# Performance work log

Hardware: AMD Instinct MI355X
Metric: run time of the kernel (lower is better)

Reference implementation:

```python
import jax, jax.numpy as jnp
import numpy as np

LMAX = 8
RES_BETA = 32   # Gauss-Legendre points in beta (>= 2*LMAX+1 -> exact quadrature for product)
RES_ALPHA = 63  # uniform points in alpha (>= 2*(2*LMAX)+1)
BATCH = 16384
DIM = (LMAX + 1) ** 2  # 81 real SH coefficients, flat index i = l*l + l + m


def _normalized_assoc_legendre(lmax, y):
    # P[b, l, m] = orthonormalized associated Legendre \bar{P}_l^m(y), 0<=m<=l,
    # normalized so that int_{-1}^{1} Pbar_l^m Pbar_l'^m dy = delta_{ll'} / (2*pi).
    n = len(y)
    P = np.zeros((n, lmax + 1, lmax + 1))
    sx = np.sqrt(np.clip(1.0 - y * y, 0.0, None))
    P[:, 0, 0] = np.sqrt(1.0 / (4.0 * np.pi))
    for m in range(1, lmax + 1):
        P[:, m, m] = -np.sqrt((2.0 * m + 1.0) / (2.0 * m)) * sx * P[:, m - 1, m - 1]
    for m in range(lmax):
        P[:, m + 1, m] = np.sqrt(2.0 * m + 3.0) * y * P[:, m, m]
    for m in range(lmax + 1):
        for l in range(m + 2, lmax + 1):
            a = np.sqrt((4.0 * l * l - 1.0) / (l * l - m * m))
            b = np.sqrt(((l - 1.0) ** 2 - m * m) / (4.0 * (l - 1.0) ** 2 - 1.0))
            P[:, l, m] = a * (y * P[:, l - 1, m] - b * P[:, l - 2, m])
    return P


def _s2grid_basis():
    # Gauss-Legendre nodes y=cos(beta) and weights (integrate sin(beta) d(beta) exactly)
    y, w = np.polynomial.legendre.leggauss(RES_BETA)
    P = _normalized_assoc_legendre(LMAX, y)
    alphas = 2.0 * np.pi * np.arange(RES_ALPHA) / RES_ALPHA
    shb = np.zeros((RES_BETA, DIM))   # Legendre part, per flat (l,m) index
    sha = np.zeros((RES_ALPHA, DIM))  # Fourier part, per flat (l,m) index
    s2 = np.sqrt(2.0)
    for l in range(LMAX + 1):
        for m in range(-l, l + 1):
            i = l * l + l + m
            shb[:, i] = P[:, l, abs(m)]
            if m == 0:
                sha[:, i] = 1.0
            elif m > 0:
                sha[:, i] = s2 * np.cos(m * alphas)
            else:
                sha[:, i] = s2 * np.sin(-m * alphas)
    qw = w * (2.0 * np.pi / RES_ALPHA)  # combined beta quadrature + alpha trapezoid weight
    return (shb.astype(np.float32), sha.astype(np.float32), qw.astype(np.float32))


def setup_inputs() -> dict:
    key = jax.random.key(0)
    k1, k2 = jax.random.split(key)
    shb, sha, qw = _s2grid_basis()
    return {
        "input1": jax.random.normal(k1, (BATCH, DIM), dtype=jnp.float32),
        "input2": jax.random.normal(k2, (BATCH, DIM), dtype=jnp.float32),
        "shb": jnp.asarray(shb),
        "sha": jnp.asarray(sha),
        "qw": jnp.asarray(qw),
    }


def _to_s2grid(x, shb, sha):
    # x: [Z, D] -> grid: [Z, res_beta, res_alpha]
    t = jnp.einsum('zi,bi->zbi', x, shb)        # Legendre expansion along beta
    return jnp.einsum('zbi,ai->zba', t, sha)    # Fourier synthesis along alpha


def _from_s2grid(g, shb, sha, qw):
    # g: [Z, res_beta, res_alpha] -> coeffs: [Z, D]
    t = jnp.einsum('zba,ai->zbi', g, sha)       # Fourier analysis along alpha
    return jnp.einsum('zbi,bi,b->zi', t, shb, qw)  # Legendre projection with quadrature


def reference(input1, input2, shb, sha, qw):
    g1 = _to_s2grid(input1, shb, sha)
    g2 = _to_s2grid(input2, shb, sha)
    return _from_s2grid(g1 * g2, shb, sha, qw)
```

## Files before the change

### kernel.cpp

```cpp
#include <hip/hip_runtime.h>

#define DIM 81
#define RA  63
#define RB  32
#define ZT  32
#define XS  104
#define OS  100

#define OFF_SHAA 0
#define OFF_SHAT 12288
#define OFF_SHBH 24576
#define OFF_SHBQ 30720
#define WS_NEED  43008

#define L_XP      43008
#define L_OB      56320
#define LDS_BYTES 69120

typedef _Float16 half8 __attribute__((ext_vector_type(8)));
typedef _Float16 half4v __attribute__((ext_vector_type(4)));
typedef __fp16  fp16x2 __attribute__((ext_vector_type(2)));
typedef float floatx16 __attribute__((ext_vector_type(16)));

union H8U { unsigned u[4]; half8 h; };
union H2U { fp16x2 h; unsigned u; };

__global__ __launch_bounds__(256) void precompute_fact(
    const float* __restrict__ shb, const float* __restrict__ sha,
    const float* __restrict__ qw, char* __restrict__ wsp)
{
    _Float16* shaAP = (_Float16*)(wsp + OFF_SHAA);
    _Float16* shaTP = (_Float16*)(wsp + OFF_SHAT);
    _Float16* shbHP = (_Float16*)(wsp + OFF_SHBH);
    float*    shbqP = (float*)(wsp + OFF_SHBQ);

    int idx = blockIdx.x * 256 + threadIdx.x;
    if (idx < 6144) {
        int j = idx & 7, lane = (idx >> 3) & 63, g = idx >> 9;
        int at = g / 6, kk = g - at * 6;
        int a = at * 32 + (lane & 31);
        int i = kk * 16 + (lane >> 5) * 8 + j;
        float v = (a < RA && i < DIM) ? sha[a * DIM + i] : 0.f;
        shaAP[idx] = (_Float16)v;
    } else if (idx < 12288) {
        int t = idx - 6144;
        int j = t & 7, lane = (t >> 3) & 63, g = t >> 9;
        int it = g >> 2, ks = g & 3;
        int a = ks * 16 + (lane >> 5) * 8 + j;
        int i = it * 32 + (lane & 31);
        float v = (a < RA && i < DIM) ? sha[a * DIM + i] : 0.f;
        shaTP[t] = (_Float16)v;
    } else if (idx < 15360) {
        int t = idx - 12288;
        int j = t & 7, hi = (t >> 3) & 1, g = t >> 4;
        int b = g / 6, kk = g - b * 6;
        int i = kk * 16 + hi * 8 + j;
        float v = (i < DIM) ? shb[b * DIM + i] : 0.f;
        shbHP[t] = (_Float16)v;
    } else if (idx < 18432) {
        int t = idx - 15360;
        int l = t & 31, g = t >> 5;
        int b = g / 3, it = g - b * 3;
        int i = it * 32 + l;
        float v = (i < DIM) ? shb[b * DIM + i] * qw[b] : 0.f;
        shbqP[t] = v;
    }
}

__global__ __launch_bounds__(512, 4) void gaunt_fact(
    const float* __restrict__ x1, const float* __restrict__ x2,
    const char* __restrict__ wsp, float* __restrict__ out)
{
    __shared__ __align__(16) char lds[LDS_BYTES];
    const _Float16* shaA_l = (const _Float16*)(lds + OFF_SHAA);
    const _Float16* shaT_l = (const _Float16*)(lds + OFF_SHAT);
    const _Float16* shbH_l = (const _Float16*)(lds + OFF_SHBH);
    const float*    shbq_l = (const float*)(lds + OFF_SHBQ);
    _Float16* xp = (_Float16*)(lds + L_XP);
    float*    ob = (float*)(lds + L_OB);

    const int tid = threadIdx.x;
    const int z0  = blockIdx.x * ZT;

    for (int i = tid; i < WS_NEED / 16; i += 512)
        ((uint4*)lds)[i] = ((const uint4*)wsp)[i];

    {
        const int nv = ZT * 24;
        #pragma unroll
        for (int in = 0; in < 2; ++in) {
            const float* src = in ? x2 : x1;
            _Float16* dst = xp + in * (ZT * XS);
            for (int idx = tid; idx < nv; idx += 512) {
                int r = idx / 24, c4 = idx - r * 24;
                float4 v = make_float4(0.f, 0.f, 0.f, 0.f);
                if (c4 < 20)       v = *(const float4*)(src + (size_t)(z0 + r) * DIM + c4 * 4);
                else if (c4 == 20) v.x = src[(size_t)(z0 + r) * DIM + 80];
                half4v h;
                h[0] = (_Float16)v.x; h[1] = (_Float16)v.y;
                h[2] = (_Float16)v.z; h[3] = (_Float16)v.w;
                *(half4v*)(dst + r * XS + c4 * 4) = h;
            }
        }
    }
    __syncthreads();

    const int l = tid & 63, l31 = l & 31, hi = l >> 5;
    const int nw = tid >> 6;

    floatx16 accO[3];
    #pragma unroll
    for (int it = 0; it < 3; ++it)
        #pragma unroll
        for (int r = 0; r < 16; ++r) accO[it][r] = 0.f;

    const _Float16* xp0 = xp + l31 * XS + hi * 8;
    const _Float16* xp1 = xp0 + ZT * XS;

    #pragma unroll 1
    for (int bi = 0; bi < 4; ++bi) {
        const int b = nw * 4 + bi;

        unsigned f[2][8];

        #pragma unroll
        for (int at = 0; at < 2; ++at) {
            floatx16 g0, g1;
            #pragma unroll
            for (int r = 0; r < 16; ++r) { g0[r] = 0.f; g1[r] = 0.f; }
            #pragma unroll
            for (int kk = 0; kk < 6; ++kk) {
                const half8 aA = *(const half8*)(shaA_l + ((at * 6 + kk) * 64 + l) * 8);
                const half8 sf = *(const half8*)(shbH_l + ((b * 6 + kk) * 2 + hi) * 8);
                const half8 aS = aA * sf;
                const half8 x0 = *(const half8*)(xp0 + kk * 16);
                const half8 x1f = *(const half8*)(xp1 + kk * 16);
                g0 = __builtin_amdgcn_mfma_f32_32x32x16_f16(aS, x0, g0, 0, 0, 0);
                g1 = __builtin_amdgcn_mfma_f32_32x32x16_f16(aS, x1f, g1, 0, 0, 0);
            }
            unsigned q[8];
            #pragma unroll
            for (int j = 0; j < 8; ++j) {
                H2U t;
                t.h = __builtin_amdgcn_cvt_pkrtz(g0[2 * j] * g1[2 * j], g0[2 * j + 1] * g1[2 * j + 1]);
                q[j] = t.u;
            }
            asm volatile("v_permlane32_swap_b32 %0, %1" : "+v"(q[0]), "+v"(q[2]));
            asm volatile("v_permlane32_swap_b32 %0, %1" : "+v"(q[1]), "+v"(q[3]));
            asm volatile("v_permlane32_swap_b32 %0, %1" : "+v"(q[4]), "+v"(q[6]));
            asm volatile("v_permlane32_swap_b32 %0, %1" : "+v"(q[5]), "+v"(q[7]));
            #pragma unroll
            for (int w = 0; w < 8; ++w) f[at][w] = q[w];
        }

        const float s0 = shbq_l[(b * 3 + 0) * 32 + l31];
        const float s1 = shbq_l[(b * 3 + 1) * 32 + l31];
        const float s2 = shbq_l[(b * 3 + 2) * 32 + l31];
        #pragma unroll
        for (int it = 0; it < 3; ++it) {
            floatx16 R;
            #pragma unroll
            for (int r = 0; r < 16; ++r) R[r] = 0.f;
            #pragma unroll
            for (int at = 0; at < 2; ++at) {
                const half8 bT0 = *(const half8*)(shaT_l + ((it * 4 + at * 2) * 64 + l) * 8);
                const half8 bT1 = *(const half8*)(shaT_l + ((it * 4 + at * 2 + 1) * 64 + l) * 8);
                H8U a0, a1;
                a0.u[0] = f[at][0]; a0.u[1] = f[at][1]; a0.u[2] = f[at][2]; a0.u[3] = f[at][3];
                a1.u[0] = f[at][4]; a1.u[1] = f[at][5]; a1.u[2] = f[at][6]; a1.u[3] = f[at][7];
                R = __builtin_amdgcn_mfma_f32_32x32x16_f16(a0.h, bT0, R, 0, 0, 0);
                R = __builtin_amdgcn_mfma_f32_32x32x16_f16(a1.h, bT1, R, 0, 0, 0);
            }
            const float s = (it == 0) ? s0 : (it == 1) ? s1 : s2;
            accO[it] += R * s;
        }
    }

    #pragma unroll 1
    for (int round = 0; round < 8; ++round) {
        __syncthreads();
        if (nw == round) {
            #pragma unroll
            for (int it = 0; it < 3; ++it)
                #pragma unroll
                for (int r = 0; r < 16; ++r) {
                    const int row = (r & 3) + 8 * (r >> 2) + 4 * hi;
                    const int col = it * 32 + l31;
                    float v = accO[it][r];
                    if (round) v += ob[row * OS + col];
                    ob[row * OS + col] = v;
                }
        }
    }
    __syncthreads();

    for (int idx = tid; idx < ZT * DIM; idx += 512) {
        int zz = idx / DIM, ii = idx - zz * DIM;
        out[(size_t)z0 * DIM + idx] = ob[zz * OS + ii];
    }
}

__device__ __forceinline__ float wave_sum64(float v) {
    v += __int_as_float(__builtin_amdgcn_update_dpp(0, __float_as_int(v), 0x111, 0xf, 0xf, true));
    v += __int_as_float(__builtin_amdgcn_update_dpp(0, __float_as_int(v), 0x112, 0xf, 0xf, true));
    v += __int_as_float(__builtin_amdgcn_update_dpp(0, __float_as_int(v), 0x114, 0xf, 0xf, true));
    v += __int_as_float(__builtin_amdgcn_update_dpp(0, __float_as_int(v), 0x118, 0xf, 0xf, true));
    v += __int_as_float(__builtin_amdgcn_update_dpp(0, __float_as_int(v), 0x142, 0xf, 0xf, true));
    v += __int_as_float(__builtin_amdgcn_update_dpp(0, __float_as_int(v), 0x143, 0xf, 0xf, true));
    return v;
}

__global__ __launch_bounds__(256) void gaunt_s2grid_kernel(
    const float* __restrict__ x1, const float* __restrict__ x2,
    const float* __restrict__ shb, const float* __restrict__ sha,
    const float* __restrict__ qw, float* __restrict__ out)
{
    __shared__ float sha_s[64 * DIM];
    __shared__ float part[4 * DIM];
    const int tid = threadIdx.x;
    const int z = blockIdx.x;
    for (int idx = tid; idx < 64 * DIM; idx += 256)
        sha_s[idx] = (idx < RA * DIM) ? sha[idx] : 0.0f;
    __syncthreads();
    const int lane = tid & 63;
    const int w = __builtin_amdgcn_readfirstlane(tid >> 6);
    const int b0 = w * 8;
    const float* xz1 = x1 + (size_t)z * DIM;
    const float* xz2 = x2 + (size_t)z * DIM;
    const float* sha_row = sha_s + lane * DIM;
    float g1[8], g2[8];
    #pragma unroll
    for (int bb = 0; bb < 8; ++bb) { g1[bb] = 0.0f; g2[bb] = 0.0f; }
    #pragma unroll 4
    for (int i = 0; i < DIM; ++i) {
        const float sv = sha_row[i];
        const float t1 = xz1[i] * sv, t2 = xz2[i] * sv;
        #pragma unroll
        for (int bb = 0; bb < 8; ++bb) {
            const float h = shb[(b0 + bb) * DIM + i];
            g1[bb] = fmaf(h, t1, g1[bb]);
            g2[bb] = fmaf(h, t2, g2[bb]);
        }
    }
    float q[8];
    #pragma unroll
    for (int bb = 0; bb < 8; ++bb) q[bb] = g1[bb] * g2[bb] * qw[b0 + bb];
    #pragma unroll 4
    for (int i = 0; i < DIM; ++i) {
        float t = 0.0f;
        #pragma unroll
        for (int bb = 0; bb < 8; ++bb) t = fmaf(q[bb], shb[(b0 + bb) * DIM + i], t);
        float v = wave_sum64(t * sha_row[i]);
        if (lane == 63) part[w * DIM + i] = v;
    }
    __syncthreads();
    for (int i = tid; i < DIM; i += 256)
        out[(size_t)z * DIM + i] = part[i] + part[DIM + i] + part[2 * DIM + i] + part[3 * DIM + i];
}

extern "C" void kernel_launch(void* const* d_in, const int* in_sizes, int n_in,
                              void* d_out, int out_size, void* d_ws, size_t ws_size,
                              hipStream_t stream) {
    const float* x1  = (const float*)d_in[0];
    const float* x2  = (const float*)d_in[1];
    const float* shb = (const float*)d_in[2];
    const float* sha = (const float*)d_in[3];
    const float* qw  = (const float*)d_in[4];
    float* out = (float*)d_out;

    const int Z = in_sizes[0] / DIM;

    if (ws_size >= WS_NEED && (Z % ZT) == 0) {
        char* wsp = (char*)d_ws;
        precompute_fact<<<72, 256, 0, stream>>>(shb, sha, qw, wsp);
        gaunt_fact<<<Z / ZT, 512, 0, stream>>>(x1, x2, wsp, out);
    } else {
        gaunt_s2grid_kernel<<<Z, 256, 0, stream>>>(x1, x2, shb, sha, qw, out);
    }
}
```

Before: 41.94 us.

## Double per-block batch tile and reuse basis fragments across two z subtiles

Raises the batch tile per block from 32 to 64 rows. Each wave now computes two 32-row subtiles, so every scaled Fourier/Legendre fragment (aS, bT) loaded from LDS feeds twice as many MFMAs, and each block's 43 KB basis copy into LDS serves twice as many rows. The output staging buffer now aliases the input buffer in LDS to keep the footprint near 69 KB. Launch bounds drop to one block per CU so the doubled accumulators fit in registers, and s_setprio is wrapped around the MFMA bursts. The trade-off is half as many blocks, which means fewer resident waves for hiding latency, plus higher register pressure.

```diff
diff --git a/kernel.cpp b/kernel.cpp
--- a/kernel.cpp
+++ b/kernel.cpp
@@ -3,7 +3,7 @@
 #define DIM 81
 #define RA  63
 #define RB  32
-#define ZT  32
+#define ZT  64
 #define XS  104
 #define OS  100
 
@@ -14,8 +14,7 @@
 #define WS_NEED  43008
 
 #define L_XP      43008
-#define L_OB      56320
-#define LDS_BYTES 69120
+#define LDS_BYTES (43008 + 26624)
 
 typedef _Float16 half8 __attribute__((ext_vector_type(8)));
 typedef _Float16 half4v __attribute__((ext_vector_type(4)));
@@ -67,7 +66,7 @@
     }
 }
 
-__global__ __launch_bounds__(512, 4) void gaunt_fact(
+__global__ __launch_bounds__(512, 1) void gaunt_fact(
     const float* __restrict__ x1, const float* __restrict__ x2,
     const char* __restrict__ wsp, float* __restrict__ out)
 {
@@ -77,7 +76,7 @@
     const _Float16* shbH_l = (const _Float16*)(lds + OFF_SHBH);
     const float*    shbq_l = (const float*)(lds + OFF_SHBQ);
     _Float16* xp = (_Float16*)(lds + L_XP);
-    float*    ob = (float*)(lds + L_OB);
+    float*    ob = (float*)(lds + L_XP);
 
     const int tid = threadIdx.x;
     const int z0  = blockIdx.x * ZT;
@@ -108,49 +107,66 @@
     const int l = tid & 63, l31 = l & 31, hi = l >> 5;
     const int nw = tid >> 6;
 
-    floatx16 accO[3];
+    const _Float16* xq00 = xp + (0 * ZT + l31) * XS + hi * 8;
+    const _Float16* xq01 = xp + (0 * ZT + 32 + l31) * XS + hi * 8;
+    const _Float16* xq10 = xp + (1 * ZT + l31) * XS + hi * 8;
+    const _Float16* xq11 = xp + (1 * ZT + 32 + l31) * XS + hi * 8;
+
+    floatx16 accO[2][3];
     #pragma unroll
-    for (int it = 0; it < 3; ++it)
-        #pragma unroll
-        for (int r = 0; r < 16; ++r) accO[it][r] = 0.f;
-
-    const _Float16* xp0 = xp + l31 * XS + hi * 8;
-    const _Float16* xp1 = xp0 + ZT * XS;
+    for (int zt = 0; zt < 2; ++zt)
+        #pragma unroll
+        for (int it = 0; it < 3; ++it)
+            #pragma unroll
+            for (int r = 0; r < 16; ++r) accO[zt][it][r] = 0.f;
 
     #pragma unroll 1
     for (int bi = 0; bi < 4; ++bi) {
         const int b = nw * 4 + bi;
 
-        unsigned f[2][8];
+        unsigned f0[2][8], f1[2][8];
 
         #pragma unroll
         for (int at = 0; at < 2; ++at) {
-            floatx16 g0, g1;
-            #pragma unroll
-            for (int r = 0; r < 16; ++r) { g0[r] = 0.f; g1[r] = 0.f; }
+            floatx16 g00, g01, g10, g11;
+            #pragma unroll
+            for (int r = 0; r < 16; ++r) { g00[r] = 0.f; g01[r] = 0.f; g10[r] = 0.f; g11[r] = 0.f; }
+            __builtin_amdgcn_s_setprio(1);
             #pragma unroll
             for (int kk = 0; kk < 6; ++kk) {
+                const half8 sf = *(const half8*)(shbH_l + ((b * 6 + kk) * 2 + hi) * 8);
                 const half8 aA = *(const half8*)(shaA_l + ((at * 6 + kk) * 64 + l) * 8);
-                const half8 sf = *(const half8*)(shbH_l + ((b * 6 + kk) * 2 + hi) * 8);
                 const half8 aS = aA * sf;
-                const half8 x0 = *(const half8*)(xp0 + kk * 16);
-                const half8 x1f = *(const half8*)(xp1 + kk * 16);
-                g0 = __builtin_amdgcn_mfma_f32_32x32x16_f16(aS, x0, g0, 0, 0, 0);
-                g1 = __builtin_amdgcn_mfma_f32_32x32x16_f16(aS, x1f, g1, 0, 0, 0);
+                const half8 x00 = *(const half8*)(xq00 + kk * 16);
+                const half8 x10 = *(const half8*)(xq10 + kk * 16);
+                const half8 x01 = *(const half8*)(xq01 + kk * 16);
+                const half8 x11 = *(const half8*)(xq11 + kk * 16);
+                g00 = __builtin_amdgcn_mfma_f32_32x32x16_f16(aS, x00, g00, 0, 0, 0);
+                g10 = __builtin_amdgcn_mfma_f32_32x32x16_f16(aS, x10, g10, 0, 0, 0);
+                g01 = __builtin_amdgcn_mfma_f32_32x32x16_f16(aS, x01, g01, 0, 0, 0);
+                g11 = __builtin_amdgcn_mfma_f32_32x32x16_f16(aS, x11, g11, 0, 0, 0);
             }
-            unsigned q[8];
+            __builtin_amdgcn_s_setprio(0);
+            floatx16 p0 = g00 * g10;
+            floatx16 p1 = g01 * g11;
+            unsigned q0[8], q1[8];
             #pragma unroll
             for (int j = 0; j < 8; ++j) {
-                H2U t;
-                t.h = __builtin_amdgcn_cvt_pkrtz(g0[2 * j] * g1[2 * j], g0[2 * j + 1] * g1[2 * j + 1]);
-                q[j] = t.u;
+                H2U t0, t1;
+                t0.h = __builtin_amdgcn_cvt_pkrtz(p0[2 * j], p0[2 * j + 1]);
+                t1.h = __builtin_amdgcn_cvt_pkrtz(p1[2 * j], p1[2 * j + 1]);
+                q0[j] = t0.u; q1[j] = t1.u;
             }
-            asm volatile("v_permlane32_swap_b32 %0, %1" : "+v"(q[0]), "+v"(q[2]));
-            asm volatile("v_permlane32_swap_b32 %0, %1" : "+v"(q[1]), "+v"(q[3]));
-            asm volatile("v_permlane32_swap_b32 %0, %1" : "+v"(q[4]), "+v"(q[6]));
-            asm volatile("v_permlane32_swap_b32 %0, %1" : "+v"(q[5]), "+v"(q[7]));
-            #pragma unroll
-            for (int w = 0; w < 8; ++w) f[at][w] = q[w];
+            asm volatile("v_permlane32_swap_b32 %0, %1" : "+v"(q0[0]), "+v"(q0[2]));
+            asm volatile("v_permlane32_swap_b32 %0, %1" : "+v"(q0[1]), "+v"(q0[3]));
+            asm volatile("v_permlane32_swap_b32 %0, %1" : "+v"(q0[4]), "+v"(q0[6]));
+            asm volatile("v_permlane32_swap_b32 %0, %1" : "+v"(q0[5]), "+v"(q0[7]));
+            asm volatile("v_permlane32_swap_b32 %0, %1" : "+v"(q1[0]), "+v"(q1[2]));
+            asm volatile("v_permlane32_swap_b32 %0, %1" : "+v"(q1[1]), "+v"(q1[3]));
+            asm volatile("v_permlane32_swap_b32 %0, %1" : "+v"(q1[4]), "+v"(q1[6]));
+            asm volatile("v_permlane32_swap_b32 %0, %1" : "+v"(q1[5]), "+v"(q1[7]));
+            #pragma unroll
+            for (int w = 0; w < 8; ++w) { f0[at][w] = q0[w]; f1[at][w] = q1[w]; }
         }
 
         const float s0 = shbq_l[(b * 3 + 0) * 32 + l31];
@@ -158,21 +174,28 @@
         const float s2 = shbq_l[(b * 3 + 2) * 32 + l31];
         #pragma unroll
         for (int it = 0; it < 3; ++it) {
-            floatx16 R;
-            #pragma unroll
-            for (int r = 0; r < 16; ++r) R[r] = 0.f;
+            floatx16 R0, R1;
+            #pragma unroll
+            for (int r = 0; r < 16; ++r) { R0[r] = 0.f; R1[r] = 0.f; }
+            __builtin_amdgcn_s_setprio(1);
             #pragma unroll
             for (int at = 0; at < 2; ++at) {
                 const half8 bT0 = *(const half8*)(shaT_l + ((it * 4 + at * 2) * 64 + l) * 8);
                 const half8 bT1 = *(const half8*)(shaT_l + ((it * 4 + at * 2 + 1) * 64 + l) * 8);
-                H8U a0, a1;
-                a0.u[0] = f[at][0]; a0.u[1] = f[at][1]; a0.u[2] = f[at][2]; a0.u[3] = f[at][3];
-                a1.u[0] = f[at][4]; a1.u[1] = f[at][5]; a1.u[2] = f[at][6]; a1.u[3] = f[at][7];
-                R = __builtin_amdgcn_mfma_f32_32x32x16_f16(a0.h, bT0, R, 0, 0, 0);
-                R = __builtin_amdgcn_mfma_f32_32x32x16_f16(a1.h, bT1, R, 0, 0, 0);
+                H8U a00, a01, a10, a11;
+                a00.u[0] = f0[at][0]; a00.u[1] = f0[at][1]; a00.u[2] = f0[at][2]; a00.u[3] = f0[at][3];
+                a01.u[0] = f0[at][4]; a01.u[1] = f0[at][5]; a01.u[2] = f0[at][6]; a01.u[3] = f0[at][7];
+                a10.u[0] = f1[at][0]; a10.u[1] = f1[at][1]; a10.u[2] = f1[at][2]; a10.u[3] = f1[at][3];
+                a11.u[0] = f1[at][4]; a11.u[1] = f1[at][5]; a11.u[2] = f1[at][6]; a11.u[3] = f1[at][7];
+                R0 = __builtin_amdgcn_mfma_f32_32x32x16_f16(a00.h, bT0, R0, 0, 0, 0);
+                R0 = __builtin_amdgcn_mfma_f32_32x32x16_f16(a01.h, bT1, R0, 0, 0, 0);
+                R1 = __builtin_amdgcn_mfma_f32_32x32x16_f16(a10.h, bT0, R1, 0, 0, 0);
+                R1 = __builtin_amdgcn_mfma_f32_32x32x16_f16(a11.h, bT1, R1, 0, 0, 0);
             }
+            __builtin_amdgcn_s_setprio(0);
             const float s = (it == 0) ? s0 : (it == 1) ? s1 : s2;
-            accO[it] += R * s;
+            accO[0][it] += R0 * s;
+            accO[1][it] += R1 * s;
         }
     }
 
@@ -181,15 +204,17 @@
         __syncthreads();
         if (nw == round) {
             #pragma unroll
-            for (int it = 0; it < 3; ++it)
+            for (int zt = 0; zt < 2; ++zt)
                 #pragma unroll
-                for (int r = 0; r < 16; ++r) {
-                    const int row = (r & 3) + 8 * (r >> 2) + 4 * hi;
-                    const int col = it * 32 + l31;
-                    float v = accO[it][r];
-                    if (round) v += ob[row * OS + col];
-                    ob[row * OS + col] = v;
-                }
+                for (int it = 0; it < 3; ++it)
+                    #pragma unroll
+                    for (int r = 0; r < 16; ++r) {
+                        const int row = zt * 32 + (r & 3) + 8 * (r >> 2) + 4 * hi;
+                        const int col = it * 32 + l31;
+                        float v = accO[zt][it][r];
+                        if (round) v += ob[row * OS + col];
+                        ob[row * OS + col] = v;
+                    }
         }
     }
     __syncthreads();
```

Result: slower. 53.23 us (+26.9%).
